# Optimization experiments

Hardware: AMD Instinct MI355X
Metric: run time of the kernel (lower is better)

Reference implementation:

```python
import jax, jax.numpy as jnp
import numpy as np

N = 50000      # nodes
E = 1_600_000  # edges (avg degree 32)
IN, H, OUT, R = 128, 64, 32, 8
NEG_SLOPE = 0.2


def _rgat(x, src, dst, etype, W, q, k, b, n_nodes):
    """PyG RGATConv, defaults: heads=1, dim=1, additive-self-attention,
    across-relation softmax, concat=True, bias=True, dropout=0 (eval)."""
    # per-relation transform of all nodes: [R, N, O] (cheaper than per-edge bmm since 2*deg >> R)
    t = jnp.einsum('ni,rio->rno', x, W)
    xi = t[etype, dst]                      # [E, O] transformed target feats
    xj = t[etype, src]                      # [E, O] transformed source feats
    a = (xi @ q + xj @ k)[:, 0]             # [E] additive attention logits
    a = jnp.where(a >= 0, a, NEG_SLOPE * a)  # leaky_relu
    # segment softmax over incoming edges of each target node (across relations)
    m = jax.ops.segment_max(a, dst, num_segments=n_nodes)
    m = jnp.where(jnp.isfinite(m), m, 0.0)
    ex = jnp.exp(a - m[dst])
    s = jax.ops.segment_sum(ex, dst, num_segments=n_nodes)
    alpha = ex / (s[dst] + 1e-16)
    out = jax.ops.segment_sum(alpha[:, None] * xj, dst, num_segments=n_nodes)
    return out + b


def setup_inputs() -> dict:
    key = jax.random.key(0)
    ks = jax.random.split(key, 24)
    x = jax.random.normal(ks[0], (N, IN), jnp.float32)
    edge_index = jax.random.randint(ks[1], (2, E), 0, N, jnp.int32)
    edge_type = jax.random.randint(ks[2], (E,), 0, R, jnp.int32)

    def glorot(k, shape, fan_in):
        return jax.random.normal(k, shape, jnp.float32) * (1.0 / np.sqrt(fan_in))

    d = dict(x=x, edge_index=edge_index, edge_type=edge_type)
    # conv1: in->hidden, conv_mu / conv_logvar: hidden->hidden
    d['W1'] = glorot(ks[3], (R, IN, H), IN)
    d['q1'] = glorot(ks[4], (H, 1), H)
    d['k1'] = glorot(ks[5], (H, 1), H)
    d['b1'] = jnp.zeros((H,), jnp.float32)
    d['Wmu'] = glorot(ks[6], (R, H, H), H)
    d['qmu'] = glorot(ks[7], (H, 1), H)
    d['kmu'] = glorot(ks[8], (H, 1), H)
    d['bmu'] = jnp.zeros((H,), jnp.float32)
    d['Wlv'] = glorot(ks[9], (R, H, H), H)
    d['qlv'] = glorot(ks[10], (H, 1), H)
    d['klv'] = glorot(ks[11], (H, 1), H)
    d['blv'] = jnp.zeros((H,), jnp.float32)
    d['Wm'] = glorot(ks[12], (H, OUT), H)   # linear_mu (stored [in,out])
    d['bm'] = jnp.zeros((OUT,), jnp.float32)
    d['Wl'] = glorot(ks[13], (H, OUT), H)   # linear_logvar
    d['bl'] = jnp.zeros((OUT,), jnp.float32)
    return d


def reference(x, edge_index, edge_type, W1, q1, k1, b1,
              Wmu, qmu, kmu, bmu, Wlv, qlv, klv, blv, Wm, bm, Wl, bl):
    src, dst = edge_index[0], edge_index[1]
    hidden = jax.nn.relu(_rgat(x, src, dst, edge_type, W1, q1, k1, b1, N))
    mu = jax.nn.relu(_rgat(hidden, src, dst, edge_type, Wmu, qmu, kmu, bmu, N))
    mu = mu @ Wm + bm                       # dropout is identity in eval
    logvar = jax.nn.relu(_rgat(hidden, src, dst, edge_type, Wlv, qlv, klv, blv, N))
    logvar = logvar @ Wl + bl
    logstd = 0.5 * logvar
    return (mu, logstd)
```

## Files before the change

### kernel.cpp

```cpp
#include <hip/hip_runtime.h>
#include <cstdint>

#define HDIM 64
#define ODIM 32
#define NEG_SLOPE 0.2f
#define SCHUNK 2048

typedef __attribute__((ext_vector_type(8))) short v8s;
typedef __attribute__((ext_vector_type(4))) float v4f;

__device__ __forceinline__ unsigned f2bf_rne(float f) {
  unsigned u = __float_as_uint(f);
  return (u + 0x7FFFu + ((u >> 16) & 1u)) >> 16;
}

__device__ __forceinline__ unsigned fenc(float f) {
  unsigned u = __float_as_uint(f);
  return (u & 0x80000000u) ? ~u : (u | 0x80000000u);
}
__device__ __forceinline__ float fdec(unsigned e) {
  unsigned u = (e & 0x80000000u) ? (e ^ 0x80000000u) : ~e;
  return __uint_as_float(u);
}

__global__ __launch_bounds__(256) void cvt_bf16_kernel(
    const float* __restrict__ in, unsigned short* __restrict__ out, int n) {
  int i = (blockIdx.x * 256 + threadIdx.x) * 4;
  if (i + 3 < n) {
    float4 v = *(const float4*)&in[i];
    ushort4 o;
    o.x = (unsigned short)f2bf_rne(v.x);
    o.y = (unsigned short)f2bf_rne(v.y);
    o.z = (unsigned short)f2bf_rne(v.z);
    o.w = (unsigned short)f2bf_rne(v.w);
    *(ushort4*)&out[i] = o;
  }
}

__global__ __launch_bounds__(256) void transpose_w_kernel(
    const float* __restrict__ W1, const float* __restrict__ Wmu,
    const float* __restrict__ Wlv, unsigned short* __restrict__ W1t,
    unsigned short* __restrict__ Wmut, unsigned short* __restrict__ Wlvt) {
  const int b = blockIdx.x;
  const int r = b & 7;
  const int which = b >> 3;
  const float* src;
  unsigned short* dst;
  int K;
  if (which == 0) {
    src = W1; dst = W1t; K = 128;
  } else if (which == 1) {
    src = Wmu; dst = Wmut; K = 64;
  } else {
    src = Wlv; dst = Wlvt; K = 64;
  }
  for (int idx = threadIdx.x; idx < K * 64; idx += 256) {
    const int kk = idx >> 6, o = idx & 63;
    dst[((size_t)r * 64 + o) * K + kk] =
        (unsigned short)f2bf_rne(src[((size_t)r * K + kk) * 64 + o]);
  }
}

__global__ __launch_bounds__(256) void count_deg_kernel(
    const int* __restrict__ dst, int* __restrict__ deg, int E) {
  int e = blockIdx.x * 256 + threadIdx.x;
  if (e < E) atomicAdd(&deg[dst[e]], 1);
}

__global__ __launch_bounds__(256) void scan_p1(const int* __restrict__ deg,
                                               int* __restrict__ bsum, int n) {
  int base = blockIdx.x * SCHUNK + threadIdx.x * 8;
  int s = 0;
#pragma unroll
  for (int j = 0; j < 8; j++) {
    int i = base + j;
    if (i < n) s += deg[i];
  }
#pragma unroll
  for (int d = 1; d < 64; d <<= 1) s += __shfl_xor(s, d, 64);
  __shared__ int ws[4];
  if ((threadIdx.x & 63) == 0) ws[threadIdx.x >> 6] = s;
  __syncthreads();
  if (threadIdx.x == 0) bsum[blockIdx.x] = ws[0] + ws[1] + ws[2] + ws[3];
}

__global__ void scan_p2(int* bsum, int nb) {
  int i = threadIdx.x;
  int v = (i < nb) ? bsum[i] : 0;
  int orig = v;
#pragma unroll
  for (int d = 1; d < 64; d <<= 1) {
    int up = __shfl_up(v, d, 64);
    if (i >= d) v += up;
  }
  if (i < nb) bsum[i] = v - orig;
}

__global__ __launch_bounds__(256) void scan_p3(const int* __restrict__ deg,
                                               const int* __restrict__ bsum,
                                               int* __restrict__ row_ptr,
                                               int n) {
  int base = blockIdx.x * SCHUNK + threadIdx.x * 8;
  int vals[8];
  int s = 0;
#pragma unroll
  for (int j = 0; j < 8; j++) {
    int i = base + j;
    vals[j] = (i < n) ? deg[i] : 0;
    s += vals[j];
  }
  int lane = threadIdx.x & 63, w = threadIdx.x >> 6;
  int v = s;
#pragma unroll
  for (int d = 1; d < 64; d <<= 1) {
    int up = __shfl_up(v, d, 64);
    if (lane >= d) v += up;
  }
  __shared__ int wsum[4];
  if (lane == 63) wsum[w] = v;
  __syncthreads();
  int woff = 0;
#pragma unroll
  for (int i = 0; i < 4; i++) woff += (i < w) ? wsum[i] : 0;
  int off = bsum[blockIdx.x] + woff + v - s;
#pragma unroll
  for (int j = 0; j < 8; j++) {
    int i = base + j;
    off += vals[j];
    if (i < n) row_ptr[i + 1] = off;
  }
  if (blockIdx.x == 0 && threadIdx.x == 0) row_ptr[0] = 0;
}

__global__ __launch_bounds__(256) void scatter_kernel(
    const int* __restrict__ src, const int* __restrict__ dst,
    const int* __restrict__ etype, const int* __restrict__ row_ptr,
    int* __restrict__ fill, int* __restrict__ edges, int E) {
  int e = blockIdx.x * 256 + threadIdx.x;
  if (e < E) {
    int d = dst[e];
    int pos = row_ptr[d] + atomicAdd(&fill[d], 1);
    edges[pos] = src[e] | (etype[e] << 16);
  }
}

__global__ __launch_bounds__(256) void rowmax_kernel(
    const float* __restrict__ ak, unsigned* __restrict__ maxk_enc, int N) {
  const int row = blockIdx.x;
  const int nchunks = gridDim.y;
  const int per = (N + nchunks - 1) / nchunks;
  const int beg = blockIdx.y * per;
  const int end = min(N, beg + per);
  const float* r = ak + (size_t)row * N;
  float m = -1e30f;
  for (int i = beg + threadIdx.x; i < end; i += 256) m = fmaxf(m, r[i]);
#pragma unroll
  for (int d = 1; d < 64; d <<= 1) m = fmaxf(m, __shfl_xor(m, d, 64));
  __shared__ float ws[4];
  if ((threadIdx.x & 63) == 0) ws[threadIdx.x >> 6] = m;
  __syncthreads();
  if (threadIdx.x == 0) {
    float bm = fmaxf(fmaxf(ws[0], ws[1]), fmaxf(ws[2], ws[3]));
    atomicMax(&maxk_enc[row], fenc(bm));
  }
}

__global__ __launch_bounds__(256) void transform1_mfma(
    const unsigned short* __restrict__ xb,
    const unsigned short* __restrict__ W1t, const float* __restrict__ q,
    const float* __restrict__ k, unsigned short* __restrict__ tb,
    float* __restrict__ aq, float* __restrict__ ak, int N) {
  __shared__ unsigned short st[4][16][72];
  const int r = blockIdx.x;
  const int tid = threadIdx.x;
  const int w = tid >> 6;
  const int lane = tid & 63;
  const int quad = lane >> 4;
  const int mrow = lane & 15;
  const int n0w = blockIdx.y * 64 + w * 16;

  const int gA = min(n0w + mrow, N - 1);
  const unsigned short* arow = xb + (size_t)gA * 128 + quad * 8;
  const unsigned short* wrow = W1t + ((size_t)r * 64 + mrow) * 128 + quad * 8;

  v4f acc[4];
#pragma unroll
  for (int tt = 0; tt < 4; tt++) acc[tt] = (v4f){0.f, 0.f, 0.f, 0.f};

#pragma unroll
  for (int k0 = 0; k0 < 128; k0 += 32) {
    v8s a = *(const v8s*)(arow + k0);
#pragma unroll
    for (int tt = 0; tt < 4; tt++) {
      v8s b = *(const v8s*)(wrow + (size_t)tt * 16 * 128 + k0);
      acc[tt] = __builtin_amdgcn_mfma_f32_16x16x32_bf16(a, b, acc[tt], 0, 0, 0);
    }
  }

  float qv[4], kv[4];
#pragma unroll
  for (int tt = 0; tt < 4; tt++) {
    qv[tt] = q[tt * 16 + mrow];
    kv[tt] = k[tt * 16 + mrow];
  }

#pragma unroll
  for (int i = 0; i < 4; i++) {
    float vq = 0.f, vk = 0.f;
#pragma unroll
    for (int tt = 0; tt < 4; tt++) {
      vq = fmaf(acc[tt][i], qv[tt], vq);
      vk = fmaf(acc[tt][i], kv[tt], vk);
      st[w][quad * 4 + i][tt * 16 + mrow] =
          (unsigned short)f2bf_rne(acc[tt][i]);
    }
#pragma unroll
    for (int d = 1; d < 16; d <<= 1) {
      vq += __shfl_xor(vq, d, 64);
      vk += __shfl_xor(vk, d, 64);
    }
    const int gn = n0w + quad * 4 + i;
    if (mrow == 0 && gn < N) {
      aq[(size_t)r * N + gn] = vq;
      ak[(size_t)r * N + gn] = vk;
    }
  }
  __syncthreads();

  const int row = lane >> 2, cg = lane & 3;
  const int gns = n0w + row;
  if (gns < N) {
    const uint4 v0 = *(const uint4*)&st[w][row][cg * 16];
    const uint4 v1 = *(const uint4*)&st[w][row][cg * 16 + 8];
    uint4* dst = (uint4*)&tb[((size_t)r * N + gns) * 64 + cg * 16];
    dst[0] = v0;
    dst[1] = v1;
  }
}

__global__ __launch_bounds__(256) void transform2_mfma(
    const unsigned short* __restrict__ hb,
    const unsigned short* __restrict__ Wmut,
    const unsigned short* __restrict__ Wlvt, const float* __restrict__ qa,
    const float* __restrict__ ka, const float* __restrict__ qb,
    const float* __restrict__ kb, unsigned* __restrict__ t2p,
    float* __restrict__ aq2, float* __restrict__ ak2, int N) {
  __shared__ unsigned st2[4][16][68];
  const int r = blockIdx.x;
  const int tid = threadIdx.x;
  const int w = tid >> 6;
  const int lane = tid & 63;
  const int quad = lane >> 4;
  const int mrow = lane & 15;
  const int n0w = blockIdx.y * 64 + w * 16;

  const int gA = min(n0w + mrow, N - 1);
  const unsigned short* arow = hb + (size_t)gA * 64 + quad * 8;
  const size_t woff = ((size_t)r * 64 + mrow) * 64 + quad * 8;

  v4f am[4], al[4];
#pragma unroll
  for (int tt = 0; tt < 4; tt++) {
    am[tt] = (v4f){0.f, 0.f, 0.f, 0.f};
    al[tt] = (v4f){0.f, 0.f, 0.f, 0.f};
  }

#pragma unroll
  for (int k0 = 0; k0 < 64; k0 += 32) {
    v8s a = *(const v8s*)(arow + k0);
#pragma unroll
    for (int tt = 0; tt < 4; tt++) {
      v8s bm = *(const v8s*)(Wmut + woff + (size_t)tt * 16 * 64 + k0);
      v8s bl = *(const v8s*)(Wlvt + woff + (size_t)tt * 16 * 64 + k0);
      am[tt] = __builtin_amdgcn_mfma_f32_16x16x32_bf16(a, bm, am[tt], 0, 0, 0);
      al[tt] = __builtin_amdgcn_mfma_f32_16x16x32_bf16(a, bl, al[tt], 0, 0, 0);
    }
  }

  float qmv[4], kmv[4], qlv2[4], klv2[4];
#pragma unroll
  for (int tt = 0; tt < 4; tt++) {
    qmv[tt] = qa[tt * 16 + mrow];
    kmv[tt] = ka[tt * 16 + mrow];
    qlv2[tt] = qb[tt * 16 + mrow];
    klv2[tt] = kb[tt * 16 + mrow];
  }

#pragma unroll
  for (int i = 0; i < 4; i++) {
    float vqm = 0.f, vkm = 0.f, vql = 0.f, vkl = 0.f;
#pragma unroll
    for (int tt = 0; tt < 4; tt++) {
      vqm = fmaf(am[tt][i], qmv[tt], vqm);
      vkm = fmaf(am[tt][i], kmv[tt], vkm);
      vql = fmaf(al[tt][i], qlv2[tt], vql);
      vkl = fmaf(al[tt][i], klv2[tt], vkl);
      st2[w][quad * 4 + i][tt * 16 + mrow] =
          f2bf_rne(am[tt][i]) | (f2bf_rne(al[tt][i]) << 16);
    }
#pragma unroll
    for (int d = 1; d < 16; d <<= 1) {
      vqm += __shfl_xor(vqm, d, 64);
      vkm += __shfl_xor(vkm, d, 64);
      vql += __shfl_xor(vql, d, 64);
      vkl += __shfl_xor(vkl, d, 64);
    }
    const int gn = n0w + quad * 4 + i;
    if (mrow == 0 && gn < N) {
      aq2[(size_t)r * N + gn] = vqm;
      ak2[(size_t)r * N + gn] = vkm;
      aq2[(size_t)(8 + r) * N + gn] = vql;
      ak2[(size_t)(8 + r) * N + gn] = vkl;
    }
  }
  __syncthreads();

  const int row = lane >> 2, cg = lane & 3;
  const int gns = n0w + row;
  if (gns < N) {
    unsigned* dst = &t2p[((size_t)r * N + gns) * 64 + cg * 16];
#pragma unroll
    for (int s = 0; s < 4; s++)
      *(uint4*)(dst + s * 4) = *(const uint4*)&st2[w][row][cg * 16 + s * 4];
  }
}

__global__ __launch_bounds__(256) void aggregate_kernel(
    const int* __restrict__ row_ptr, const int* __restrict__ edges,
    const unsigned short* __restrict__ tb, const float* __restrict__ aq,
    const float* __restrict__ ak, const unsigned* __restrict__ maxk_enc,
    const float* __restrict__ bias, unsigned short* __restrict__ hb, int N) {
  const int tid = threadIdx.x;
  const int w = tid >> 6, o = tid & 63;
  int wid = blockIdx.x * 4 + w;
  const bool valid = wid < N;
  if (!valid) wid = N - 1;
  const int beg = row_ptr[wid];
  const int end = valid ? row_ptr[wid + 1] : beg;
  const int deg = end - beg;

  const float aqw = aq[(size_t)(o & 7) * N + wid];

  float v = aqw + fdec(maxk_enc[o & 7]);
  v = (v >= 0.f) ? v : NEG_SLOPE * v;
#pragma unroll
  for (int d = 1; d < 8; d <<= 1) v = fmaxf(v, __shfl_xor(v, d, 64));
  const float m = __shfl(v, 0, 64);

  float s = 0.f, acc = 0.f;
  for (int base = 0; base < deg; base += 64) {
    const int j = base + o;
    const int gcount = min(64, deg - base);
    const int packed = edges[beg + min(j, deg - 1)];
    const int src = packed & 0xFFFF;
    const int rr = packed >> 16;
    const int idx = rr * N + src;
    float x = __shfl(aqw, rr, 64) + ak[idx];
    x = (x >= 0.f) ? x : NEG_SLOPE * x;
    const float p = (j < deg) ? __expf(x - m) : 0.f;
    s += p;
    const int g8 = (gcount + 7) & ~7;
    for (int u = 0; u < g8; u += 8) {
      float pu[8];
      int iu[8];
#pragma unroll
      for (int q = 0; q < 8; q++) {
        pu[q] = __shfl(p, u + q, 64);
        iu[q] = __shfl(idx, u + q, 64);
      }
      unsigned short tv[8];
#pragma unroll
      for (int q = 0; q < 8; q++) tv[q] = tb[(size_t)iu[q] * 64 + o];
#pragma unroll
      for (int q = 0; q < 8; q++)
        acc = fmaf(pu[q], __uint_as_float((unsigned)tv[q] << 16), acc);
    }
  }
#pragma unroll
  for (int d = 1; d < 64; d <<= 1) s += __shfl_xor(s, d, 64);

  if (valid) {
    const float res = acc / (s + 1e-16f) + bias[o];
    hb[(size_t)wid * 64 + o] = (unsigned short)f2bf_rne(fmaxf(res, 0.f));
  }
}

__global__ __launch_bounds__(256) void aggregate2_kernel(
    const int* __restrict__ row_ptr, const int* __restrict__ edges,
    const unsigned* __restrict__ t2p, const float* __restrict__ aq2,
    const float* __restrict__ ak2, const unsigned* __restrict__ maxk2_enc,
    const float* __restrict__ bmu, const float* __restrict__ blv,
    const float* __restrict__ Wm, const float* __restrict__ bm,
    const float* __restrict__ Wlin, const float* __restrict__ bl,
    float* __restrict__ out_mu, float* __restrict__ out_ls, int N) {
  __shared__ float WmL[2048];
  __shared__ float WlL[2048];
  __shared__ float bL[64];
  __shared__ float hL[4][130];
  const int tid = threadIdx.x;
  for (int i = tid; i < 2048; i += 256) {
    WmL[i] = Wm[i];
    WlL[i] = Wlin[i];
  }
  if (tid < 32) {
    bL[tid] = bm[tid];
    bL[32 + tid] = bl[tid];
  }
  __syncthreads();

  const int w = tid >> 6, o = tid & 63;
  int wid = blockIdx.x * 4 + w;
  const bool valid = wid < N;
  if (!valid) wid = N - 1;
  const int beg = row_ptr[wid];
  const int end = valid ? row_ptr[wid + 1] : beg;
  const int deg = end - beg;

  const float aqw = aq2[(size_t)(o & 15) * N + wid];

  float v = aqw + fdec(maxk2_enc[o & 15]);
  v = (v >= 0.f) ? v : NEG_SLOPE * v;
#pragma unroll
  for (int d = 1; d < 8; d <<= 1) v = fmaxf(v, __shfl_xor(v, d, 64));
  const float m0 = __shfl(v, 0, 64);
  const float m1 = __shfl(v, 8, 64);

  float s0 = 0.f, s1 = 0.f, acc0 = 0.f, acc1 = 0.f;
  for (int base = 0; base < deg; base += 64) {
    const int j = base + o;
    const int gcount = min(64, deg - base);
    const int packed = edges[beg + min(j, deg - 1)];
    const int src = packed & 0xFFFF;
    const int rr = packed >> 16;
    const int idx = rr * N + src;
    float x0 = __shfl(aqw, rr, 64) + ak2[idx];
    float x1 = __shfl(aqw, 8 + rr, 64) + ak2[idx + 8 * N];
    x0 = (x0 >= 0.f) ? x0 : NEG_SLOPE * x0;
    x1 = (x1 >= 0.f) ? x1 : NEG_SLOPE * x1;
    const float p0 = (j < deg) ? __expf(x0 - m0) : 0.f;
    const float p1 = (j < deg) ? __expf(x1 - m1) : 0.f;
    s0 += p0;
    s1 += p1;
    const int g8 = (gcount + 7) & ~7;
    for (int u = 0; u < g8; u += 8) {
      float pu0[8], pu1[8];
      int iu[8];
#pragma unroll
      for (int q = 0; q < 8; q++) {
        pu0[q] = __shfl(p0, u + q, 64);
        pu1[q] = __shfl(p1, u + q, 64);
        iu[q] = __shfl(idx, u + q, 64);
      }
      unsigned pk[8];
#pragma unroll
      for (int q = 0; q < 8; q++) pk[q] = t2p[(size_t)iu[q] * 64 + o];
#pragma unroll
      for (int q = 0; q < 8; q++) {
        acc0 = fmaf(pu0[q], __uint_as_float(pk[q] << 16), acc0);
        acc1 = fmaf(pu1[q], __uint_as_float(pk[q] & 0xFFFF0000u), acc1);
      }
    }
  }
#pragma unroll
  for (int d = 1; d < 64; d <<= 1) {
    s0 += __shfl_xor(s0, d, 64);
    s1 += __shfl_xor(s1, d, 64);
  }

  const float h0 = fmaxf(acc0 / (s0 + 1e-16f) + bmu[o], 0.f);
  const float h1 = fmaxf(acc1 / (s1 + 1e-16f) + blv[o], 0.f);
  hL[w][o] = h0;
  hL[w][64 + o] = h1;
  __syncthreads();

  const float* hrow = &hL[w][(o >= 32) ? 64 : 0];
  const float* WL = (o >= 32) ? WlL : WmL;
  const int j = o & 31;
  float acc = 0.f;
#pragma unroll 8
  for (int c = 0; c < 64; c++) acc = fmaf(hrow[c], WL[c * 32 + j], acc);
  if (valid) {
    if (o < 32)
      out_mu[(size_t)wid * 32 + j] = acc + bL[j];
    else
      out_ls[(size_t)wid * 32 + j] = (acc + bL[32 + j]) * 0.5f;
  }
}

extern "C" void kernel_launch(void* const* d_in, const int* in_sizes, int n_in,
                              void* d_out, int out_size, void* d_ws,
                              size_t ws_size, hipStream_t stream) {
  const float* x = (const float*)d_in[0];
  const int* edge_index = (const int*)d_in[1];
  const int* edge_type = (const int*)d_in[2];
  const float* W1 = (const float*)d_in[3];
  const float* q1 = (const float*)d_in[4];
  const float* k1 = (const float*)d_in[5];
  const float* b1 = (const float*)d_in[6];
  const float* Wmu = (const float*)d_in[7];
  const float* qmu = (const float*)d_in[8];
  const float* kmu = (const float*)d_in[9];
  const float* bmu = (const float*)d_in[10];
  const float* Wlv = (const float*)d_in[11];
  const float* qlv = (const float*)d_in[12];
  const float* klv = (const float*)d_in[13];
  const float* blv = (const float*)d_in[14];
  const float* Wm = (const float*)d_in[15];
  const float* bm = (const float*)d_in[16];
  const float* Wl = (const float*)d_in[17];
  const float* bl = (const float*)d_in[18];

  const int N = in_sizes[0] / 128;
  const int E = in_sizes[2];
  const int R = in_sizes[3] / (128 * 64);

  float* out_mu = (float*)d_out;
  float* out_ls = (float*)d_out + (size_t)N * ODIM;

  char* wsp = (char*)d_ws;
  size_t off = 0;
  auto carve = [&](size_t bytes) {
    void* p = wsp + off;
    off += (bytes + 255) & ~(size_t)255;
    return p;
  };

  void* tbuf = carve((size_t)R * N * 64 * sizeof(unsigned));
  unsigned short* t1b = (unsigned short*)tbuf;
  unsigned* t2p = (unsigned*)tbuf;
  unsigned short* xb = (unsigned short*)carve((size_t)N * 128 * 2);
  unsigned short* hb = (unsigned short*)carve((size_t)N * 64 * 2);
  unsigned short* W1t = (unsigned short*)carve((size_t)R * 64 * 128 * 2);
  unsigned short* Wmut = (unsigned short*)carve((size_t)R * 64 * 64 * 2);
  unsigned short* Wlvt = (unsigned short*)carve((size_t)R * 64 * 64 * 2);
  float* aq2 = (float*)carve((size_t)2 * R * N * sizeof(float));
  float* ak2 = (float*)carve((size_t)2 * R * N * sizeof(float));
  unsigned* maxk_enc = (unsigned*)carve(2 * R * sizeof(unsigned));
  int* deg = (int*)carve((size_t)N * sizeof(int));
  int* fill = (int*)carve((size_t)N * sizeof(int));
  int* row_ptr = (int*)carve((size_t)(N + 1) * sizeof(int));
  int* bsum = (int*)carve(256 * sizeof(int));
  int* edges = (int*)carve((size_t)E * sizeof(int));

  const int* e_src = edge_index;
  const int* e_dst = edge_index + E;

  cvt_bf16_kernel<<<(N * 128 / 4 + 255) / 256, 256, 0, stream>>>(x, xb,
                                                                 N * 128);
  transpose_w_kernel<<<3 * R, 256, 0, stream>>>(W1, Wmu, Wlv, W1t, Wmut, Wlvt);

  hipMemsetAsync(deg, 0, (size_t)N * sizeof(int), stream);
  hipMemsetAsync(fill, 0, (size_t)N * sizeof(int), stream);
  hipMemsetAsync(maxk_enc, 0, 2 * R * sizeof(unsigned), stream);
  count_deg_kernel<<<(E + 255) / 256, 256, 0, stream>>>(e_dst, deg, E);
  const int nchunk = (N + SCHUNK - 1) / SCHUNK;
  scan_p1<<<nchunk, 256, 0, stream>>>(deg, bsum, N);
  scan_p2<<<1, 64, 0, stream>>>(bsum, nchunk);
  scan_p3<<<nchunk, 256, 0, stream>>>(deg, bsum, row_ptr, N);
  scatter_kernel<<<(E + 255) / 256, 256, 0, stream>>>(e_src, e_dst, edge_type,
                                                      row_ptr, fill, edges, E);

  const int nb64 = (N + 63) / 64;
  const int agg_blocks = (N + 3) / 4;

  transform1_mfma<<<dim3(R, nb64), 256, 0, stream>>>(xb, W1t, q1, k1, t1b,
                                                     aq2, ak2, N);
  rowmax_kernel<<<dim3(R, 32), 256, 0, stream>>>(ak2, maxk_enc, N);
  aggregate_kernel<<<agg_blocks, 256, 0, stream>>>(
      row_ptr, edges, t1b, aq2, ak2, maxk_enc, b1, hb, N);

  hipMemsetAsync(maxk_enc, 0, 2 * R * sizeof(unsigned), stream);

  transform2_mfma<<<dim3(R, nb64), 256, 0, stream>>>(
      hb, Wmut, Wlvt, qmu, kmu, qlv, klv, t2p, aq2, ak2, N);
  rowmax_kernel<<<dim3(2 * R, 32), 256, 0, stream>>>(ak2, maxk_enc, N);
  aggregate2_kernel<<<agg_blocks, 256, 0, stream>>>(
      row_ptr, edges, t2p, aq2, ak2, maxk_enc, bmu, blv, Wm, bm, Wl, bl,
      out_mu, out_ls, N);
}
```

Baseline: 617.2 us.

## Replace global-atomic CSR scatter with two-pass bucketed counting sort

The single scatter kernel, which used a global atomic per edge and wrote to random addresses, is replaced by a two-pass bucket sort. Pass one histograms each 8192-edge chunk into 256-row buckets in shared memory and reserves space with per-bucket global atomics. It then stages the records in LDS and writes them out in bucket-contiguous runs. Pass two has each block read its bucket's contiguous range and place edges into final CSR slots using shared-memory atomics, which should give more coalesced writes and fewer global atomics, at the cost of an extra E-sized temporary buffer and two more launches.

```diff
diff --git a/kernel.cpp b/kernel.cpp
--- a/kernel.cpp
+++ b/kernel.cpp
@@ -5,6 +5,7 @@
 #define ODIM 32
 #define NEG_SLOPE 0.2f
 #define SCHUNK 2048
+#define EPB 8192
 
 typedef __attribute__((ext_vector_type(8))) short v8s;
 typedef __attribute__((ext_vector_type(4))) float v4f;
@@ -132,15 +133,88 @@
   if (blockIdx.x == 0 && threadIdx.x == 0) row_ptr[0] = 0;
 }
 
-__global__ __launch_bounds__(256) void scatter_kernel(
+__global__ __launch_bounds__(256) void bucket_cursor_init(
+    const int* __restrict__ row_ptr, int* __restrict__ cursor, int N, int nb) {
+  int i = threadIdx.x;
+  if (i < nb) cursor[i] = row_ptr[min(i * 256, N)];
+}
+
+__global__ __launch_bounds__(256) void bucket_pass1(
     const int* __restrict__ src, const int* __restrict__ dst,
-    const int* __restrict__ etype, const int* __restrict__ row_ptr,
-    int* __restrict__ fill, int* __restrict__ edges, int E) {
-  int e = blockIdx.x * 256 + threadIdx.x;
-  if (e < E) {
-    int d = dst[e];
-    int pos = row_ptr[d] + atomicAdd(&fill[d], 1);
-    edges[pos] = src[e] | (etype[e] << 16);
+    const int* __restrict__ etype, int* __restrict__ cursor,
+    unsigned* __restrict__ tmp, int E) {
+  __shared__ int hist[256];
+  __shared__ int binstart[256];
+  __shared__ int gbase[256];
+  __shared__ int fill[256];
+  __shared__ int wsum[4];
+  __shared__ unsigned stage[EPB];
+  __shared__ unsigned char binof[EPB];
+  const int tid = threadIdx.x;
+  const int e0 = blockIdx.x * EPB;
+  const int cnt = min(EPB, E - e0);
+
+  hist[tid] = 0;
+  fill[tid] = 0;
+  __syncthreads();
+  for (int j = tid; j < cnt; j += 256) atomicAdd(&hist[dst[e0 + j] >> 8], 1);
+  __syncthreads();
+
+  const int hv = hist[tid];
+  {
+    const int lane = tid & 63, w = tid >> 6;
+    int iv = hv;
+#pragma unroll
+    for (int d = 1; d < 64; d <<= 1) {
+      int up = __shfl_up(iv, d, 64);
+      if (lane >= d) iv += up;
+    }
+    if (lane == 63) wsum[w] = iv;
+    __syncthreads();
+    int woff = 0;
+#pragma unroll
+    for (int i = 0; i < 4; i++) woff += (i < w) ? wsum[i] : 0;
+    binstart[tid] = woff + iv - hv;
+    if (hv > 0) gbase[tid] = atomicAdd(&cursor[tid], hv);
+  }
+  __syncthreads();
+
+  for (int j = tid; j < cnt; j += 256) {
+    const int d = dst[e0 + j];
+    const int b = d >> 8;
+    const unsigned rec = ((unsigned)(d & 255) << 19) |
+                         ((unsigned)etype[e0 + j] << 16) |
+                         (unsigned)src[e0 + j];
+    const int slot = binstart[b] + atomicAdd(&fill[b], 1);
+    stage[slot] = rec;
+    binof[slot] = (unsigned char)b;
+  }
+  __syncthreads();
+
+  for (int s = tid; s < cnt; s += 256) {
+    const int b = binof[s];
+    tmp[gbase[b] + (s - binstart[b])] = stage[s];
+  }
+}
+
+__global__ __launch_bounds__(256) void bucket_pass2(
+    const int* __restrict__ row_ptr, const unsigned* __restrict__ tmp,
+    int* __restrict__ edges, int N) {
+  __shared__ int rp[257];
+  __shared__ int fill[256];
+  const int tid = threadIdx.x;
+  const int rowbase = blockIdx.x * 256;
+  const int rowcnt = min(256, N - rowbase);
+  for (int i = tid; i <= rowcnt; i += 256) rp[i] = row_ptr[rowbase + i];
+  fill[tid] = 0;
+  __syncthreads();
+  const int beg = rp[0];
+  const int endv = rp[rowcnt];
+  for (int i = beg + tid; i < endv; i += 256) {
+    const unsigned rec = tmp[i];
+    const int dlow = rec >> 19;
+    const int pos = rp[dlow] + atomicAdd(&fill[dlow], 1);
+    edges[pos] = (int)(rec & 0x7FFFFu);
   }
 }
 
@@ -537,9 +611,10 @@
   float* ak2 = (float*)carve((size_t)2 * R * N * sizeof(float));
   unsigned* maxk_enc = (unsigned*)carve(2 * R * sizeof(unsigned));
   int* deg = (int*)carve((size_t)N * sizeof(int));
-  int* fill = (int*)carve((size_t)N * sizeof(int));
   int* row_ptr = (int*)carve((size_t)(N + 1) * sizeof(int));
   int* bsum = (int*)carve(256 * sizeof(int));
+  int* cursor = (int*)carve(256 * sizeof(int));
+  unsigned* tmp = (unsigned*)carve((size_t)E * sizeof(unsigned));
   int* edges = (int*)carve((size_t)E * sizeof(int));
 
   const int* e_src = edge_index;
@@ -550,15 +625,19 @@
   transpose_w_kernel<<<3 * R, 256, 0, stream>>>(W1, Wmu, Wlv, W1t, Wmut, Wlvt);
 
   hipMemsetAsync(deg, 0, (size_t)N * sizeof(int), stream);
-  hipMemsetAsync(fill, 0, (size_t)N * sizeof(int), stream);
   hipMemsetAsync(maxk_enc, 0, 2 * R * sizeof(unsigned), stream);
   count_deg_kernel<<<(E + 255) / 256, 256, 0, stream>>>(e_dst, deg, E);
   const int nchunk = (N + SCHUNK - 1) / SCHUNK;
   scan_p1<<<nchunk, 256, 0, stream>>>(deg, bsum, N);
   scan_p2<<<1, 64, 0, stream>>>(bsum, nchunk);
   scan_p3<<<nchunk, 256, 0, stream>>>(deg, bsum, row_ptr, N);
-  scatter_kernel<<<(E + 255) / 256, 256, 0, stream>>>(e_src, e_dst, edge_type,
-                                                      row_ptr, fill, edges, E);
+
+  const int nbuck = (N + 255) >> 8;
+  bucket_cursor_init<<<1, 256, 0, stream>>>(row_ptr, cursor, N, nbuck);
+  bucket_pass1<<<(E + EPB - 1) / EPB, 256, 0, stream>>>(e_src, e_dst,
+                                                        edge_type, cursor,
+                                                        tmp, E);
+  bucket_pass2<<<nbuck, 256, 0, stream>>>(row_ptr, tmp, edges, N);
 
   const int nb64 = (N + 63) / 64;
   const int agg_blocks = (N + 3) / 4;
```

Measured after the change: 563.0 us. -8.8%, faster.
